# Performance work log

Measured on AMD Instinct MI355X. Metric: run time of the kernel, lower is better.

## Reference

```python
import jax, jax.numpy as jnp
import numpy as np

N_NODES = 10000
NUM_FEAT = 128
HIDD = 256
HEADS = 8
NUM_CLASS = 10
NEG_SLOPE = 0.2


def _gat_conv(x, src, dst, W, att_src, att_dst, bias, n_nodes):
    # x: [N, F_in]; W: [F_in, H*C]; att_*: [H, C]; bias: [H*C]
    H, C = att_src.shape
    h = (x @ W).reshape(n_nodes, H, C)                      # [N, H, C]
    a_src = jnp.einsum('nhc,hc->nh', h, att_src)            # [N, H]
    a_dst = jnp.einsum('nhc,hc->nh', h, att_dst)            # [N, H]
    e = a_src[src] + a_dst[dst]                             # [E, H]
    e = jnp.where(e >= 0, e, NEG_SLOPE * e)                 # leaky_relu
    # segment softmax over edges grouped by destination node
    e_max = jax.ops.segment_max(jax.lax.stop_gradient(e), dst, num_segments=n_nodes)
    e_max = jnp.where(jnp.isfinite(e_max), e_max, 0.0)
    ex = jnp.exp(e - e_max[dst])                            # [E, H]
    denom = jax.ops.segment_sum(ex, dst, num_segments=n_nodes)
    alpha = ex / (denom[dst] + 1e-16)                       # [E, H]
    msg = h[src] * alpha[:, :, None]                        # [E, H, C]
    out = jax.ops.segment_sum(msg, dst, num_segments=n_nodes)
    return out.reshape(n_nodes, H * C) + bias


def setup_inputs() -> dict:
    key = jax.random.key(0)
    ks = jax.random.split(key, 12)
    x = jax.random.normal(ks[0], (N_NODES, NUM_FEAT), dtype=jnp.float32)
    edge_index = jax.random.randint(ks[1], (2, 50000), 0, N_NODES, dtype=jnp.int64)
    g1 = 1.0 / np.sqrt(NUM_FEAT)
    g2 = 1.0 / np.sqrt(HEADS * HIDD)
    return {
        'x': x,
        'edge_index': edge_index,
        'W1': jax.random.normal(ks[2], (NUM_FEAT, HEADS * HIDD), dtype=jnp.float32) * g1,
        'att_src1': jax.random.normal(ks[3], (HEADS, HIDD), dtype=jnp.float32) * g2,
        'att_dst1': jax.random.normal(ks[4], (HEADS, HIDD), dtype=jnp.float32) * g2,
        'b1': jnp.zeros((HEADS * HIDD,), dtype=jnp.float32),
        'W2': jax.random.normal(ks[5], (HEADS * HIDD, NUM_CLASS), dtype=jnp.float32) * g2,
        'att_src2': jax.random.normal(ks[6], (1, NUM_CLASS), dtype=jnp.float32),
        'att_dst2': jax.random.normal(ks[7], (1, NUM_CLASS), dtype=jnp.float32),
        'b2': jnp.zeros((NUM_CLASS,), dtype=jnp.float32),
    }


def reference(x, edge_index, W1, att_src1, att_dst1, b1, W2, att_src2, att_dst2, b2):
    n = x.shape[0]
    # PyG GATConv default add_self_loops=True
    loop = jnp.arange(n, dtype=edge_index.dtype)
    src = jnp.concatenate([edge_index[0], loop])
    dst = jnp.concatenate([edge_index[1], loop])
    h = _gat_conv(x, src, dst, W1, att_src1, att_dst1, b1, n)
    h = jax.nn.elu(h)
    h = _gat_conv(h, src, dst, W2, att_src2, att_dst2, b2, n)
    return jax.nn.sigmoid(h)
```

## Files before the change

### kernel.cpp

```cpp
#include <hip/hip_runtime.h>
#include <math.h>

#define N_NODES 10000
#define N_PAD   10112
#define NPB     632
#define E0      50000
#define E_TOT   60000
#define FIN     128
#define HEADS   8
#define CHN     256
#define HC      2048
#define NC      10
#define NEG     0.2f
#define MAXD    128
#define MAXD2   64

typedef __attribute__((ext_vector_type(8))) short bf16x8;
typedef __attribute__((ext_vector_type(4))) float f32x4;


__device__ __forceinline__ unsigned f2u(float f){
  unsigned u = __float_as_uint(f);
  return (u & 0x80000000u) ? ~u : (u | 0x80000000u);
}
__device__ __forceinline__ float u2f(unsigned u){
  return __uint_as_float((u & 0x80000000u) ? (u & 0x7fffffffu) : ~u);
}
__device__ __forceinline__ unsigned short bf16_rne(float f){
  unsigned u = __float_as_uint(f);
  return (unsigned short)((u + 0x7FFFu + ((u >> 16) & 1u)) >> 16);
}

__global__ void k_init(const int* __restrict__ raw, int* __restrict__ flag,
                       int* __restrict__ deg, int* __restrict__ cursor){
  int t = blockIdx.x*256 + threadIdx.x;
  if (t < N_NODES){ deg[t] = 0; cursor[t] = 0; }
  if (blockIdx.x == 0 && threadIdx.x < 64){
    int i = threadIdx.x;
    bool bad = (raw[2*i + 1] != 0) || ((unsigned)raw[2*i] >= (unsigned)N_NODES);
    unsigned long long b = __ballot(bad);
    if (i == 0) *flag = (b == 0ull) ? 1 : 0;
  }
}

__global__ void k_convert(const int* __restrict__ raw, const int* __restrict__ flag,
                          int* __restrict__ esrc, int* __restrict__ edst,
                          int* __restrict__ deg){
  int e = blockIdx.x * blockDim.x + threadIdx.x;
  if (e >= E_TOT) return;
  int s, d;
  if (e < E0){
    if (*flag){ s = raw[2*e]; d = raw[2*(E0 + e)]; }
    else      { s = raw[e];   d = raw[E0 + e];     }
  } else {
    s = d = e - E0;
  }
  esrc[e] = s; edst[e] = d;
  atomicAdd(&deg[d], 1);
}

__global__ __launch_bounds__(256) void k_prepw(const float* __restrict__ W1,
                                               const float* __restrict__ att_src,
                                               const float* __restrict__ att_dst,
                                               unsigned short* __restrict__ w1t_hi,
                                               unsigned short* __restrict__ w1t_lo,
                                               float* __restrict__ vv){
  int t = blockIdx.x*256 + threadIdx.x;
  {
    int k = t >> 11;
    int n = t & 2047;
    float v = W1[(size_t)k*HC + n];
    unsigned short hi = bf16_rne(v);
    float hf = __uint_as_float((unsigned)hi << 16);
    unsigned short lo = bf16_rne(v - hf);
    int cb = n >> 4, c = n & 15, klin = k >> 3, j = k & 7;
    size_t idx = (size_t)cb*2048 + klin*128 + c*8 + j;
    w1t_hi[idx] = hi;
    w1t_lo[idx] = lo;
  }
  if (t < FIN*HEADS){
    int k = t >> 3, h = t & 7;
    const float* wrow = W1 + (size_t)k*HC + h*CHN;
    const float* as   = att_src + h*CHN;
    const float* ad   = att_dst + h*CHN;
    float s = 0.f, d = 0.f;
    #pragma unroll 4
    for (int c = 0; c < CHN; c += 4){
      float4 w = *reinterpret_cast<const float4*>(wrow + c);
      float4 a = *reinterpret_cast<const float4*>(as + c);
      float4 b = *reinterpret_cast<const float4*>(ad + c);
      s += w.x*a.x + w.y*a.y + w.z*a.z + w.w*a.w;
      d += w.x*b.x + w.y*b.y + w.z*b.z + w.w*b.w;
    }
    vv[k*16 + h]     = s;
    vv[k*16 + 8 + h] = d;
  }
}

__global__ __launch_bounds__(256) void k_attdot(const float* __restrict__ x,
                                                const float* __restrict__ vv,
                                                float* __restrict__ a_src,
                                                float* __restrict__ a_dst){
  const int wave = threadIdx.x >> 6, lane = threadIdx.x & 63;
  const int n = blockIdx.x*4 + wave;
  const int u = lane & 15, c = lane >> 4;
  const float* xr = x + (size_t)n*FIN + c*32;
  float acc = 0.f;
  #pragma unroll
  for (int q = 0; q < 8; ++q){
    float4 xv = *reinterpret_cast<const float4*>(xr + q*4);
    int k = c*32 + q*4;
    acc = fmaf(xv.x, vv[(k+0)*16 + u], acc);
    acc = fmaf(xv.y, vv[(k+1)*16 + u], acc);
    acc = fmaf(xv.z, vv[(k+2)*16 + u], acc);
    acc = fmaf(xv.w, vv[(k+3)*16 + u], acc);
  }
  acc += __shfl_xor(acc, 16);
  acc += __shfl_xor(acc, 32);
  if (c == 0){
    if (u < 8) a_src[n*HEADS + u] = acc;
    else       a_dst[n*HEADS + (u - 8)] = acc;
  }
}

__global__ __launch_bounds__(1024) void k_scan(const int* __restrict__ deg,
                                               int* __restrict__ offs){
  __shared__ int sums[1024];
  const int tid = threadIdx.x;
  int base = tid*10;
  int vals[10];
  int local = 0;
  #pragma unroll
  for (int i = 0; i < 10; ++i){
    int idx = base + i;
    int v = (idx < N_NODES) ? deg[idx] : 0;
    vals[i] = local;
    local += v;
  }
  sums[tid] = local;
  __syncthreads();
  for (int o = 1; o < 1024; o <<= 1){
    int t = (tid >= o) ? sums[tid - o] : 0;
    __syncthreads();
    sums[tid] += t;
    __syncthreads();
  }
  int boff = (tid == 0) ? 0 : sums[tid - 1];
  #pragma unroll
  for (int i = 0; i < 10; ++i){
    int idx = base + i;
    if (idx < N_NODES) offs[idx] = boff + vals[i];
  }
  if (tid == 1023) offs[N_NODES] = sums[1023];
}

__global__ void k_scatter(const int* __restrict__ esrc, const int* __restrict__ edst,
                          const int* __restrict__ offs, int* __restrict__ cursor,
                          int* __restrict__ csr_src){
  int e = blockIdx.x*256 + threadIdx.x;
  if (e < E_TOT){
    int d = edst[e];
    int pos = offs[d] + atomicAdd(&cursor[d], 1);
    csr_src[pos] = esrc[e];
  }
}

__global__ __launch_bounds__(128) void k_aggx(const float* __restrict__ x,
                                              const float* __restrict__ a_src1,
                                              const float* __restrict__ a_dst1,
                                              const int* __restrict__ offs,
                                              const int* __restrict__ csr_src,
                                              unsigned short* __restrict__ agg_hi,
                                              unsigned short* __restrict__ agg_lo){
  __shared__ float s_e[MAXD][HEADS];
  __shared__ int s_src[MAXD];
  __shared__ unsigned s_maxu[HEADS];
  __shared__ float s_sum[HEADS];
  __shared__ float s_inv[HEADS];
  __shared__ float s_ad[HEADS];
  const int n = blockIdx.x, tid = threadIdx.x;
  const int start = offs[n];
  int deg = offs[n+1] - start;
  if (deg > MAXD) deg = MAXD;
  if (tid < HEADS){
    s_maxu[tid] = 0u;
    s_sum[tid] = 0.f;
    s_ad[tid] = a_dst1[n*HEADS + tid];
  }
  for (int i = tid; i < deg; i += 128) s_src[i] = csr_src[start + i];
  __syncthreads();
  const int tot = deg*HEADS;
  for (int i = tid; i < tot; i += 128){
    int e = i >> 3, hh = i & 7;
    float v = a_src1[s_src[e]*HEADS + hh] + s_ad[hh];
    v = (v >= 0.f) ? v : NEG*v;
    s_e[e][hh] = v;
    atomicMax(&s_maxu[hh], f2u(v));
  }
  __syncthreads();
  for (int i = tid; i < tot; i += 128){
    int e = i >> 3, hh = i & 7;
    float v = expf(s_e[e][hh] - u2f(s_maxu[hh]));
    s_e[e][hh] = v;
    atomicAdd(&s_sum[hh], v);
  }
  __syncthreads();
  if (tid < HEADS) s_inv[tid] = 1.f/(s_sum[tid] + 1e-16f);
  __syncthreads();
  for (int i = tid; i < tot; i += 128) s_e[i>>3][i&7] *= s_inv[i&7];
  __syncthreads();
  float acc[HEADS] = {0,0,0,0,0,0,0,0};
  for (int e = 0; e < deg; ++e){
    float xv = x[(size_t)s_src[e]*FIN + tid];
    #pragma unroll
    for (int h = 0; h < HEADS; ++h) acc[h] = fmaf(s_e[e][h], xv, acc[h]);
  }
  const int rb = n >> 4, r = n & 15;
  const int koff = (tid >> 3)*128 + r*8 + (tid & 7);
  #pragma unroll
  for (int h = 0; h < HEADS; ++h){
    float v = acc[h];
    unsigned short hi = bf16_rne(v);
    float hf = __uint_as_float((unsigned)hi << 16);
    unsigned short lo = bf16_rne(v - hf);
    size_t idx = ((size_t)h*NPB + rb)*2048 + koff;
    agg_hi[idx] = hi;
    agg_lo[idx] = lo;
  }
}

__global__ __launch_bounds__(256) void k_gemm1(const unsigned short* __restrict__ agg_hi,
                                               const unsigned short* __restrict__ agg_lo,
                                               const unsigned short* __restrict__ w1t_hi,
                                               const unsigned short* __restrict__ w1t_lo,
                                               const float* __restrict__ b1,
                                               float* __restrict__ out1){
  const int tid = threadIdx.x;
  const int bx = blockIdx.x;
  const int by = blockIdx.y;
  const int h  = bx >> 1;
  const int wave = tid >> 6, lane = tid & 63;
  const int wr = wave >> 1, wc = wave & 1;
  const int nl = lane & 15, g = lane >> 4;
  const int colb = bx*128 + wc*64;
  const int lelem = lane*8;

  f32x4 zero4 = {0.f, 0.f, 0.f, 0.f};
  f32x4 acc[4][4];
  #pragma unroll
  for (int fm = 0; fm < 4; ++fm)
    #pragma unroll
    for (int fn = 0; fn < 4; ++fn) acc[fm][fn] = zero4;

  const size_t arb0 = (size_t)h*NPB + by*8 + wr*4;
  const size_t brb0 = (size_t)bx*8 + wc*4;

  #pragma unroll
  for (int ch = 0; ch < 2; ++ch){
    #pragma unroll
    for (int s = 0; s < 2; ++s){
      const int koff = (ch*8 + s*4)*128 + lelem;
      bf16x8 ah[4], al[4];
      #pragma unroll
      for (int fm = 0; fm < 4; ++fm){
        size_t ao = (arb0 + fm)*2048 + koff;
        ah[fm] = *reinterpret_cast<const bf16x8*>(agg_hi + ao);
        al[fm] = *reinterpret_cast<const bf16x8*>(agg_lo + ao);
      }
      #pragma unroll
      for (int fn = 0; fn < 4; ++fn){
        size_t bo = (brb0 + fn)*2048 + koff;
        bf16x8 bh = *reinterpret_cast<const bf16x8*>(w1t_hi + bo);
        bf16x8 bl = *reinterpret_cast<const bf16x8*>(w1t_lo + bo);
        #pragma unroll
        for (int fm = 0; fm < 4; ++fm){
          acc[fm][fn] = __builtin_amdgcn_mfma_f32_16x16x32_bf16(ah[fm], bh, acc[fm][fn], 0, 0, 0);
          acc[fm][fn] = __builtin_amdgcn_mfma_f32_16x16x32_bf16(ah[fm], bl, acc[fm][fn], 0, 0, 0);
          acc[fm][fn] = __builtin_amdgcn_mfma_f32_16x16x32_bf16(al[fm], bh, acc[fm][fn], 0, 0, 0);
        }
      }
    }
  }

  #pragma unroll
  for (int fm = 0; fm < 4; ++fm){
    #pragma unroll
    for (int fn = 0; fn < 4; ++fn){
      int col = colb + fn*16 + nl;
      float bb = b1[col];
      #pragma unroll
      for (int r = 0; r < 4; ++r){
        int row = by*128 + wr*64 + fm*16 + g*4 + r;
        if (row < N_NODES){
          float v = acc[fm][fn][r] + bb;
          v = (v > 0.f) ? v : (__expf(v) - 1.f);
          out1[(size_t)row*HC + col] = v;
        }
      }
    }
  }
}

__global__ __launch_bounds__(256) void k_gemv2(const float* __restrict__ out1,
                                               const float* __restrict__ W2,
                                               const float* __restrict__ as2,
                                               const float* __restrict__ ad2,
                                               float* __restrict__ h2,
                                               float* __restrict__ a_src2,
                                               float* __restrict__ a_dst2){
  __shared__ float W2s[256][13];
  const int tid = threadIdx.x;
  const int nl = tid & 15;
  const int ng = tid >> 4;
  const int n = blockIdx.x*16 + ng;
  float acc[NC];
  #pragma unroll
  for (int j = 0; j < NC; ++j) acc[j] = 0.f;
  const float* row = out1 + (size_t)n*HC;
  for (int c = 0; c < 8; ++c){
    if (c) __syncthreads();
    {
      const float2* src = reinterpret_cast<const float2*>(W2 + (size_t)(c*256 + tid)*NC);
      #pragma unroll
      for (int q = 0; q < 5; ++q){
        float2 w = src[q];
        W2s[tid][2*q]   = w.x;
        W2s[tid][2*q+1] = w.y;
      }
    }
    __syncthreads();
    #pragma unroll
    for (int i = 0; i < 4; ++i){
      int kq = i*64 + nl*4;
      float4 v = *reinterpret_cast<const float4*>(row + c*256 + kq);
      float vm[4] = {v.x, v.y, v.z, v.w};
      #pragma unroll
      for (int m = 0; m < 4; ++m){
        const float* wrow = &W2s[kq + m][0];
        #pragma unroll
        for (int j = 0; j < NC; ++j)
          acc[j] = fmaf(vm[m], wrow[j], acc[j]);
      }
    }
  }
  #pragma unroll
  for (int o = 1; o < 16; o <<= 1){
    #pragma unroll
    for (int j = 0; j < NC; ++j) acc[j] += __shfl_xor(acc[j], o);
  }
  if (nl == 0){
    float ds = 0.f, dd = 0.f;
    #pragma unroll
    for (int j = 0; j < NC; ++j){
      h2[(size_t)n*NC + j] = acc[j];
      ds = fmaf(acc[j], as2[j], ds);
      dd = fmaf(acc[j], ad2[j], dd);
    }
    a_src2[n] = ds;
    a_dst2[n] = dd;
  }
}

__global__ __launch_bounds__(64) void k_agg2(const float* __restrict__ h2,
                                             const float* __restrict__ a_src2,
                                             const float* __restrict__ a_dst2,
                                             const int* __restrict__ offs,
                                             const int* __restrict__ csr_src,
                                             const float* __restrict__ b2,
                                             float* __restrict__ out){
  __shared__ float s_al[MAXD2];
  __shared__ int s_sc[MAXD2];
  const int n = blockIdx.x, lane = threadIdx.x;
  const int start = offs[n];
  int deg = offs[n+1] - start;
  if (deg > MAXD2) deg = MAXD2;
  const float ad = a_dst2[n];
  float e = -INFINITY;
  if (lane < deg){
    int src = csr_src[start + lane];
    s_sc[lane] = src;
    e = a_src2[src] + ad;
    e = (e >= 0.f) ? e : NEG*e;
  }
  float m = e;
  #pragma unroll
  for (int o = 1; o < 64; o <<= 1) m = fmaxf(m, __shfl_xor(m, o));
  float ex = (lane < deg) ? expf(e - m) : 0.f;
  float s = ex;
  #pragma unroll
  for (int o = 1; o < 64; o <<= 1) s += __shfl_xor(s, o);
  if (lane < deg) s_al[lane] = ex / (s + 1e-16f);
  __syncthreads();
  if (lane < NC){
    float acc = 0.f;
    for (int i = 0; i < deg; ++i)
      acc = fmaf(s_al[i], h2[(size_t)s_sc[i]*NC + lane], acc);
    float v = acc + b2[lane];
    out[n*NC + lane] = 1.f/(1.f + expf(-v));
  }
}

extern "C" void kernel_launch(void* const* d_in, const int* in_sizes, int n_in,
                              void* d_out, int out_size, void* d_ws, size_t ws_size,
                              hipStream_t stream){
  const float* x   = (const float*)d_in[0];
  const int*   ei  = (const int*)  d_in[1];
  const float* W1  = (const float*)d_in[2];
  const float* as1 = (const float*)d_in[3];
  const float* ad1 = (const float*)d_in[4];
  const float* b1  = (const float*)d_in[5];
  const float* W2  = (const float*)d_in[6];
  const float* as2 = (const float*)d_in[7];
  const float* ad2 = (const float*)d_in[8];
  const float* b2  = (const float*)d_in[9];
  float* out = (float*)d_out;

  char* ws = (char*)d_ws;
  size_t off = 0;
  auto alloc = [&](size_t bytes) -> void* {
    void* p = ws + off;
    off += (bytes + 255) & ~(size_t)255;
    return p;
  };
  float* out1    = (float*)alloc((size_t)N_NODES*HC*4);
  unsigned short* agg_hi = (unsigned short*)alloc((size_t)HEADS*N_PAD*FIN*2);
  unsigned short* agg_lo = (unsigned short*)alloc((size_t)HEADS*N_PAD*FIN*2);
  unsigned short* w1t_hi = (unsigned short*)alloc((size_t)HC*FIN*2);
  unsigned short* w1t_lo = (unsigned short*)alloc((size_t)HC*FIN*2);
  float* vv      = (float*)alloc((size_t)FIN*16*4);
  float* a_src1  = (float*)alloc((size_t)N_NODES*HEADS*4);
  float* a_dst1  = (float*)alloc((size_t)N_NODES*HEADS*4);
  float* h2      = (float*)alloc((size_t)N_NODES*NC*4);
  float* a_src2  = (float*)alloc((size_t)N_NODES*4);
  float* a_dst2  = (float*)alloc((size_t)N_NODES*4);
  int*   deg     = (int*)alloc((size_t)N_NODES*4);
  int*   offs    = (int*)alloc((size_t)(N_NODES+1)*4);
  int*   cursor  = (int*)alloc((size_t)N_NODES*4);
  int*   esrc    = (int*)alloc((size_t)E_TOT*4);
  int*   edst    = (int*)alloc((size_t)E_TOT*4);
  int*   csr_src = (int*)alloc((size_t)E_TOT*4);
  int*   flag    = (int*)alloc(4);
  (void)ws_size; (void)in_sizes; (void)n_in; (void)out_size;

  k_init   <<<40, 256, 0, stream>>>(ei, flag, deg, cursor);
  k_convert<<<(E_TOT + 255)/256, 256, 0, stream>>>(ei, flag, esrc, edst, deg);
  k_prepw  <<<(HC*FIN)/256, 256, 0, stream>>>(W1, as1, ad1, w1t_hi, w1t_lo, vv);
  k_attdot <<<N_NODES/4, 256, 0, stream>>>(x, vv, a_src1, a_dst1);
  k_scan   <<<1, 1024, 0, stream>>>(deg, offs);
  k_scatter<<<(E_TOT + 255)/256, 256, 0, stream>>>(esrc, edst, offs, cursor, csr_src);
  k_aggx   <<<N_NODES, 128, 0, stream>>>(x, a_src1, a_dst1, offs, csr_src, agg_hi, agg_lo);
  k_gemm1  <<<dim3(16, N_PAD/128), 256, 0, stream>>>(agg_hi, agg_lo, w1t_hi, w1t_lo, b1, out1);
  k_gemv2  <<<N_NODES/16, 256, 0, stream>>>(out1, W2, as2, ad2, h2, a_src2, a_dst2);
  k_agg2   <<<N_NODES, 64, 0, stream>>>(h2, a_src2, a_dst2, offs, csr_src, b2, out);
}
```

Measured before the change: 239.6 us.

## Fuse layer-2 projection into GEMM1 epilogue with atomic partial sums

The second-layer projection (ELU output times W2) now runs inside the GEMM1 epilogue. Each block multiplies its accumulator tile by a shared-memory slice of W2, reduces across lanes with shuffles, and atomically adds partial results into h2, which is zeroed in k_init. This removes the 80MB round trip of the out1 intermediate and the separate GEMV kernel, replacing them with a small attention-dot kernel. It also reorders the operand loads to issue before the MFMAs. The cost is many float atomics, higher register pressure and nondeterministic summation order.

```diff
diff --git a/kernel.cpp b/kernel.cpp
--- a/kernel.cpp
+++ b/kernel.cpp
@@ -32,9 +32,11 @@
 }
 
 __global__ void k_init(const int* __restrict__ raw, int* __restrict__ flag,
-                       int* __restrict__ deg, int* __restrict__ cursor){
+                       int* __restrict__ deg, int* __restrict__ cursor,
+                       float* __restrict__ h2){
   int t = blockIdx.x*256 + threadIdx.x;
   if (t < N_NODES){ deg[t] = 0; cursor[t] = 0; }
+  for (int i = t; i < N_NODES*NC; i += 40*256) h2[i] = 0.f;
   if (blockIdx.x == 0 && threadIdx.x < 64){
     int i = threadIdx.x;
     bool bad = (raw[2*i + 1] != 0) || ((unsigned)raw[2*i] >= (unsigned)N_NODES);
@@ -234,16 +236,24 @@
                                                const unsigned short* __restrict__ w1t_hi,
                                                const unsigned short* __restrict__ w1t_lo,
                                                const float* __restrict__ b1,
-                                               float* __restrict__ out1){
+                                               const float* __restrict__ W2,
+                                               float* __restrict__ h2){
+  __shared__ float W2s[128][13];
   const int tid = threadIdx.x;
   const int bx = blockIdx.x;
   const int by = blockIdx.y;
   const int h  = bx >> 1;
+  const int colbase = bx*128;
   const int wave = tid >> 6, lane = tid & 63;
   const int wr = wave >> 1, wc = wave & 1;
   const int nl = lane & 15, g = lane >> 4;
-  const int colb = bx*128 + wc*64;
+  const int colb = colbase + wc*64;
   const int lelem = lane*8;
+
+  for (int i = tid; i < 128*NC; i += 256){
+    int c = i/NC, j = i - c*NC;
+    W2s[c][j] = W2[(size_t)(colbase + c)*NC + j];
+  }
 
   f32x4 zero4 = {0.f, 0.f, 0.f, 0.f};
   f32x4 acc[4][4];
@@ -257,108 +267,87 @@
 
   #pragma unroll
   for (int ch = 0; ch < 2; ++ch){
+    bf16x8 ah[2][4], al[2][4], bh[2][4], bl[2][4];
     #pragma unroll
     for (int s = 0; s < 2; ++s){
       const int koff = (ch*8 + s*4)*128 + lelem;
-      bf16x8 ah[4], al[4];
-      #pragma unroll
-      for (int fm = 0; fm < 4; ++fm){
-        size_t ao = (arb0 + fm)*2048 + koff;
-        ah[fm] = *reinterpret_cast<const bf16x8*>(agg_hi + ao);
-        al[fm] = *reinterpret_cast<const bf16x8*>(agg_lo + ao);
+      #pragma unroll
+      for (int f = 0; f < 4; ++f){
+        ah[s][f] = *reinterpret_cast<const bf16x8*>(agg_hi + (arb0 + f)*2048 + koff);
+        al[s][f] = *reinterpret_cast<const bf16x8*>(agg_lo + (arb0 + f)*2048 + koff);
+        bh[s][f] = *reinterpret_cast<const bf16x8*>(w1t_hi + (brb0 + f)*2048 + koff);
+        bl[s][f] = *reinterpret_cast<const bf16x8*>(w1t_lo + (brb0 + f)*2048 + koff);
       }
-      #pragma unroll
-      for (int fn = 0; fn < 4; ++fn){
-        size_t bo = (brb0 + fn)*2048 + koff;
-        bf16x8 bh = *reinterpret_cast<const bf16x8*>(w1t_hi + bo);
-        bf16x8 bl = *reinterpret_cast<const bf16x8*>(w1t_lo + bo);
+    }
+    #pragma unroll
+    for (int s = 0; s < 2; ++s)
+      #pragma unroll
+      for (int fn = 0; fn < 4; ++fn)
         #pragma unroll
         for (int fm = 0; fm < 4; ++fm){
-          acc[fm][fn] = __builtin_amdgcn_mfma_f32_16x16x32_bf16(ah[fm], bh, acc[fm][fn], 0, 0, 0);
-          acc[fm][fn] = __builtin_amdgcn_mfma_f32_16x16x32_bf16(ah[fm], bl, acc[fm][fn], 0, 0, 0);
-          acc[fm][fn] = __builtin_amdgcn_mfma_f32_16x16x32_bf16(al[fm], bh, acc[fm][fn], 0, 0, 0);
+          acc[fm][fn] = __builtin_amdgcn_mfma_f32_16x16x32_bf16(ah[s][fm], bh[s][fn], acc[fm][fn], 0, 0, 0);
+          acc[fm][fn] = __builtin_amdgcn_mfma_f32_16x16x32_bf16(ah[s][fm], bl[s][fn], acc[fm][fn], 0, 0, 0);
+          acc[fm][fn] = __builtin_amdgcn_mfma_f32_16x16x32_bf16(al[s][fm], bh[s][fn], acc[fm][fn], 0, 0, 0);
         }
+  }
+
+  #pragma unroll
+  for (int fn = 0; fn < 4; ++fn){
+    float bb = b1[colb + fn*16 + nl];
+    #pragma unroll
+    for (int fm = 0; fm < 4; ++fm)
+      #pragma unroll
+      for (int r = 0; r < 4; ++r){
+        float v = acc[fm][fn][r] + bb;
+        acc[fm][fn][r] = (v > 0.f) ? v : (__expf(v) - 1.f);
+      }
+  }
+  __syncthreads();
+
+  #pragma unroll
+  for (int fm = 0; fm < 4; ++fm){
+    #pragma unroll
+    for (int r = 0; r < 4; ++r){
+      int row = by*128 + wr*64 + fm*16 + g*4 + r;
+      float p[NC];
+      #pragma unroll
+      for (int j = 0; j < NC; ++j) p[j] = 0.f;
+      #pragma unroll
+      for (int fn = 0; fn < 4; ++fn){
+        float e = acc[fm][fn][r];
+        const float* w = &W2s[wc*64 + fn*16 + nl][0];
+        #pragma unroll
+        for (int j = 0; j < NC; ++j) p[j] = fmaf(e, w[j], p[j]);
+      }
+      #pragma unroll
+      for (int o = 1; o < 16; o <<= 1){
+        #pragma unroll
+        for (int j = 0; j < NC; ++j) p[j] += __shfl_xor(p[j], o);
+      }
+      if (nl == 0 && row < N_NODES){
+        #pragma unroll
+        for (int j = 0; j < NC; ++j) atomicAdd(&h2[(size_t)row*NC + j], p[j]);
       }
     }
   }
-
-  #pragma unroll
-  for (int fm = 0; fm < 4; ++fm){
-    #pragma unroll
-    for (int fn = 0; fn < 4; ++fn){
-      int col = colb + fn*16 + nl;
-      float bb = b1[col];
-      #pragma unroll
-      for (int r = 0; r < 4; ++r){
-        int row = by*128 + wr*64 + fm*16 + g*4 + r;
-        if (row < N_NODES){
-          float v = acc[fm][fn][r] + bb;
-          v = (v > 0.f) ? v : (__expf(v) - 1.f);
-          out1[(size_t)row*HC + col] = v;
-        }
-      }
-    }
-  }
-}
-
-__global__ __launch_bounds__(256) void k_gemv2(const float* __restrict__ out1,
-                                               const float* __restrict__ W2,
-                                               const float* __restrict__ as2,
-                                               const float* __restrict__ ad2,
-                                               float* __restrict__ h2,
-                                               float* __restrict__ a_src2,
-                                               float* __restrict__ a_dst2){
-  __shared__ float W2s[256][13];
-  const int tid = threadIdx.x;
-  const int nl = tid & 15;
-  const int ng = tid >> 4;
-  const int n = blockIdx.x*16 + ng;
-  float acc[NC];
-  #pragma unroll
-  for (int j = 0; j < NC; ++j) acc[j] = 0.f;
-  const float* row = out1 + (size_t)n*HC;
-  for (int c = 0; c < 8; ++c){
-    if (c) __syncthreads();
-    {
-      const float2* src = reinterpret_cast<const float2*>(W2 + (size_t)(c*256 + tid)*NC);
-      #pragma unroll
-      for (int q = 0; q < 5; ++q){
-        float2 w = src[q];
-        W2s[tid][2*q]   = w.x;
-        W2s[tid][2*q+1] = w.y;
-      }
-    }
-    __syncthreads();
-    #pragma unroll
-    for (int i = 0; i < 4; ++i){
-      int kq = i*64 + nl*4;
-      float4 v = *reinterpret_cast<const float4*>(row + c*256 + kq);
-      float vm[4] = {v.x, v.y, v.z, v.w};
-      #pragma unroll
-      for (int m = 0; m < 4; ++m){
-        const float* wrow = &W2s[kq + m][0];
-        #pragma unroll
-        for (int j = 0; j < NC; ++j)
-          acc[j] = fmaf(vm[m], wrow[j], acc[j]);
-      }
-    }
-  }
-  #pragma unroll
-  for (int o = 1; o < 16; o <<= 1){
-    #pragma unroll
-    for (int j = 0; j < NC; ++j) acc[j] += __shfl_xor(acc[j], o);
-  }
-  if (nl == 0){
-    float ds = 0.f, dd = 0.f;
-    #pragma unroll
-    for (int j = 0; j < NC; ++j){
-      h2[(size_t)n*NC + j] = acc[j];
-      ds = fmaf(acc[j], as2[j], ds);
-      dd = fmaf(acc[j], ad2[j], dd);
-    }
-    a_src2[n] = ds;
-    a_dst2[n] = dd;
-  }
+}
+
+__global__ __launch_bounds__(256) void k_h2dots(const float* __restrict__ h2,
+                                                const float* __restrict__ as2,
+                                                const float* __restrict__ ad2,
+                                                float* __restrict__ a_src2,
+                                                float* __restrict__ a_dst2){
+  int n = blockIdx.x*256 + threadIdx.x;
+  if (n >= N_NODES) return;
+  float ds = 0.f, dd = 0.f;
+  #pragma unroll
+  for (int j = 0; j < NC; ++j){
+    float v = h2[(size_t)n*NC + j];
+    ds = fmaf(v, as2[j], ds);
+    dd = fmaf(v, ad2[j], dd);
+  }
+  a_src2[n] = ds;
+  a_dst2[n] = dd;
 }
 
 __global__ __launch_bounds__(64) void k_agg2(const float* __restrict__ h2,
@@ -422,7 +411,6 @@
     off += (bytes + 255) & ~(size_t)255;
     return p;
   };
-  float* out1    = (float*)alloc((size_t)N_NODES*HC*4);
   unsigned short* agg_hi = (unsigned short*)alloc((size_t)HEADS*N_PAD*FIN*2);
   unsigned short* agg_lo = (unsigned short*)alloc((size_t)HEADS*N_PAD*FIN*2);
   unsigned short* w1t_hi = (unsigned short*)alloc((size_t)HC*FIN*2);
@@ -442,14 +430,14 @@
   int*   flag    = (int*)alloc(4);
   (void)ws_size; (void)in_sizes; (void)n_in; (void)out_size;
 
-  k_init   <<<40, 256, 0, stream>>>(ei, flag, deg, cursor);
+  k_init   <<<40, 256, 0, stream>>>(ei, flag, deg, cursor, h2);
   k_convert<<<(E_TOT + 255)/256, 256, 0, stream>>>(ei, flag, esrc, edst, deg);
   k_prepw  <<<(HC*FIN)/256, 256, 0, stream>>>(W1, as1, ad1, w1t_hi, w1t_lo, vv);
   k_attdot <<<N_NODES/4, 256, 0, stream>>>(x, vv, a_src1, a_dst1);
   k_scan   <<<1, 1024, 0, stream>>>(deg, offs);
   k_scatter<<<(E_TOT + 255)/256, 256, 0, stream>>>(esrc, edst, offs, cursor, csr_src);
   k_aggx   <<<N_NODES, 128, 0, stream>>>(x, a_src1, a_dst1, offs, csr_src, agg_hi, agg_lo);
-  k_gemm1  <<<dim3(16, N_PAD/128), 256, 0, stream>>>(agg_hi, agg_lo, w1t_hi, w1t_lo, b1, out1);
-  k_gemv2  <<<N_NODES/16, 256, 0, stream>>>(out1, W2, as2, ad2, h2, a_src2, a_dst2);
+  k_gemm1  <<<dim3(16, N_PAD/128), 256, 0, stream>>>(agg_hi, agg_lo, w1t_hi, w1t_lo, b1, W2, h2);
+  k_h2dots <<<(N_NODES + 255)/256, 256, 0, stream>>>(h2, as2, ad2, a_src2, a_dst2);
   k_agg2   <<<N_NODES, 64, 0, stream>>>(h2, a_src2, a_dst2, offs, csr_src, b2, out);
 }
```

Result: slower. 423.9 us (+76.9%).
